# Performance work log

Measured on AMD Instinct MI355X. Metric: run time of the kernel, lower is better.

The kernel has to match this reference:

```python
import jax, jax.numpy as jnp
import numpy as np

N_NODES = 100000
N_EDGES = 3200000
C, H, F = 512, 256, 64


def spmm(edge_row, edge_col, edge_val, Z):
    # (A @ Z)[i] = sum over edges e with row[e]==i of val[e] * Z[col[e]]
    msgs = edge_val[:, None] * Z[edge_col]  # [E, d]
    return jax.ops.segment_sum(msgs, edge_row, num_segments=N_NODES)


def setup_inputs() -> dict:
    key = jax.random.key(0)
    k1, k2, k3, k4, k5, k6, k7 = jax.random.split(key, 7)
    X = jax.random.normal(k1, (N_NODES, C), dtype=jnp.float32)
    edge_row = jax.random.randint(k2, (N_EDGES,), 0, N_NODES, dtype=jnp.int32)
    edge_col = jax.random.randint(k3, (N_EDGES,), 0, N_NODES, dtype=jnp.int32)
    edge_val = jax.random.uniform(k4, (N_EDGES,), dtype=jnp.float32)
    W0 = jax.random.normal(k5, (C, H), dtype=jnp.float32) * (C ** -0.5)
    Wh1 = jax.random.normal(k6, (H, H), dtype=jnp.float32) * (H ** -0.5)
    W1 = jax.random.normal(k7, (H, F), dtype=jnp.float32) * (H ** -0.5)
    return {"X": X, "edge_row": edge_row, "edge_col": edge_col,
            "edge_val": edge_val, "W0": W0, "Wh1": Wh1, "W1": W1}


def reference(X, edge_row, edge_col, edge_val, W0, Wh1, W1):
    # layer 0: relu(A @ (X W0))   (dropout=0 -> identity)
    Z = jax.nn.relu(spmm(edge_row, edge_col, edge_val, X @ W0))
    # hidden layers (num_layers - 2 = 1)
    Z = jax.nn.relu(spmm(edge_row, edge_col, edge_val, Z @ Wh1))
    # output layer: softmax(A @ (Z W1), axis=-1)
    Z = jax.nn.softmax(spmm(edge_row, edge_col, edge_val, Z @ W1), axis=-1)
    return Z
```

## Files before the change

### kernel.cpp

```cpp
#include <hip/hip_runtime.h>
#include <cstdint>
#include <cstddef>


#define SCAN_B 1024

typedef __attribute__((ext_vector_type(8))) short short8_t;
typedef __attribute__((ext_vector_type(4))) short short4_t;
typedef __attribute__((ext_vector_type(4))) float f32x4;

__device__ __forceinline__ short bf16_hi(float x) {
    union { float f; unsigned u; } c; c.f = x;
    return (short)(c.u >> 16);
}
__device__ __forceinline__ float bf16_f32(short h) {
    union { float f; unsigned u; } c; c.u = ((unsigned)(unsigned short)h) << 16;
    return c.f;
}

__device__ __forceinline__ void gload_lds16(const void* g, void* l) {
    __builtin_amdgcn_global_load_lds(
        (const __attribute__((address_space(1))) void*)g,
        (__attribute__((address_space(3))) void*)l, 16, 0, 0);
}


__global__ void count_rows_k(const int* __restrict__ row, int* __restrict__ deg, int E) {
    int e = blockIdx.x * blockDim.x + threadIdx.x;
    if (e < E) atomicAdd(&deg[row[e]], 1);
}

__global__ __launch_bounds__(SCAN_B) void scan1_k(const int* __restrict__ deg,
                                                  int* __restrict__ part,
                                                  int* __restrict__ bsum, int n) {
    __shared__ int buf[SCAN_B];
    int tid = threadIdx.x;
    int i = blockIdx.x * SCAN_B + tid;
    int v = (i < n) ? ((deg[i] + 3) & ~3) : 0;
    buf[tid] = v;
    __syncthreads();
    for (int off = 1; off < SCAN_B; off <<= 1) {
        int y = (tid >= off) ? buf[tid - off] : 0;
        __syncthreads();
        buf[tid] += y;
        __syncthreads();
    }
    if (i < n) part[i] = buf[tid] - v;
    if (tid == SCAN_B - 1) bsum[blockIdx.x] = buf[tid];
}

__global__ __launch_bounds__(128) void scan2_k(int* __restrict__ bsum, int nb) {
    __shared__ int buf[128];
    int tid = threadIdx.x;
    int v = (tid < nb) ? bsum[tid] : 0;
    buf[tid] = v;
    __syncthreads();
    for (int off = 1; off < 128; off <<= 1) {
        int y = (tid >= off) ? buf[tid - off] : 0;
        __syncthreads();
        buf[tid] += y;
        __syncthreads();
    }
    if (tid < nb) bsum[tid] = buf[tid] - v;
    if (tid == nb - 1) bsum[nb] = buf[tid];
}

__global__ __launch_bounds__(SCAN_B) void scan3_k(int* __restrict__ rowptr,
                                                  const int* __restrict__ bsum,
                                                  int* __restrict__ cursor, int n, int nb) {
    int i = blockIdx.x * SCAN_B + threadIdx.x;
    if (i < n) {
        int v = rowptr[i] + bsum[blockIdx.x];
        rowptr[i] = v;
        cursor[i] = v;
    }
    if (i == 0) rowptr[n] = bsum[nb];
}

__global__ __launch_bounds__(256) void scatter_xcd_k(const int* __restrict__ row,
                                                     const int* __restrict__ col,
                                                     const float* __restrict__ val,
                                                     int* __restrict__ cursor,
                                                     int2* __restrict__ ecv,
                                                     int E, int gsz) {
    const int g = blockIdx.x & 7;
    const int rank = blockIdx.x >> 3;
    const int R = gridDim.x >> 3;
    const int lo = g * gsz, hi = lo + gsz;
    for (int e = rank * 256 + threadIdx.x; e < E; e += R * 256) {
        int r = row[e];
        if (r >= lo && r < hi) {
            int p = atomicAdd(&cursor[r], 1);
            ecv[p] = make_int2(col[e], __float_as_int(val[e]));
        }
    }
}


__global__ void split_w_k(const float* __restrict__ W, short* __restrict__ Bhl,
                          int K, int M) {
    int i = blockIdx.x * 256 + threadIdx.x;
    if (i >= K * M) return;
    int k = i / M, m = i - k * M;
    float x = W[i];
    short hi = bf16_hi(x);
    float r = x - bf16_f32(hi);
    short lo = bf16_hi(r);
    int g = k >> 3, j = k & 7;
    Bhl[(size_t)m * (2 * K) + 16 * g + j] = hi;
    Bhl[(size_t)m * (2 * K) + 16 * g + 8 + j] = lo;
}


template <int K, int BN, int NWR, int NWC, bool AF32>
__global__ __launch_bounds__(256) void gemm_hl(const void* __restrict__ Av,
                                               const short* __restrict__ Bhl,
                                               short* __restrict__ ZQ,
                                               float* __restrict__ scl, int N) {
    constexpr int BM = 64 * NWR;
    constexpr int NF = BN / NWC / 16;
    constexpr int NT = K / 32;
    __shared__ short Ald[2][BM * 64];
    __shared__ short Bld[2][BN * 64];

    const int tid = threadIdx.x, lane = tid & 63, w = tid >> 6;
    const int wr = w / NWC, wc = w % NWC;
    const int row0 = blockIdx.x * BM;
    const int l8 = lane >> 3;
    const int sx = (lane & 7) ^ l8;

    const short* Ahl = (const short*)Av;
    const float* Af  = (const float*)Av;
    const int arow = tid >> 2, aq = tid & 3;
    const int akey = arow & 7;

    f32x4 acc[4][NF] = {};

    auto stageB = [&](int t, int b) {
#pragma unroll
        for (int ch = w; ch < BN / 8; ch += 4)
            gload_lds16(Bhl + (size_t)(ch * 8 + l8) * (2 * K) + (size_t)t * 64 + sx * 8,
                        &Bld[b][ch * 512]);
    };
    auto stageAg = [&](int t, int b) {
#pragma unroll
        for (int ch = w; ch < BM / 8; ch += 4)
            gload_lds16(Ahl + (size_t)(row0 + ch * 8 + l8) * (2 * K) + (size_t)t * 64 + sx * 8,
                        &Ald[b][ch * 512]);
    };
    auto loadAf = [&](int t, float4& x0, float4& x1) {
        int gr = row0 + arow;
        x0 = make_float4(0.f, 0.f, 0.f, 0.f); x1 = x0;
        if (gr < N) {
            x0 = *(const float4*)&Af[(size_t)gr * K + t * 32 + aq * 8];
            x1 = *(const float4*)&Af[(size_t)gr * K + t * 32 + aq * 8 + 4];
        }
    };
    auto writeAf = [&](int b, float4 x0, float4 x1) {
        float f[8] = {x0.x, x0.y, x0.z, x0.w, x1.x, x1.y, x1.z, x1.w};
        short8_t hi, lo;
#pragma unroll
        for (int j = 0; j < 8; ++j) {
            short hh = bf16_hi(f[j]);
            hi[j] = hh;
            lo[j] = bf16_hi(f[j] - bf16_f32(hh));
        }
        *(short8_t*)&Ald[b][arow * 64 + ((2 * aq) ^ akey) * 8] = hi;
        *(short8_t*)&Ald[b][arow * 64 + ((2 * aq + 1) ^ akey) * 8] = lo;
    };

    if constexpr (AF32) {
        float4 x0, x1;
        loadAf(0, x0, x1);
        writeAf(0, x0, x1);
    } else {
        stageAg(0, 0);
    }
    stageB(0, 0);
    __syncthreads();

    for (int t = 0; t < NT; ++t) {
        const int cur = t & 1, nxt = cur ^ 1;
        float4 px0, px1;
        if (t + 1 < NT) {
            if constexpr (AF32) loadAf(t + 1, px0, px1);
            else                stageAg(t + 1, nxt);
            stageB(t + 1, nxt);
        }

        const int sH = (lane >> 4) * 2, sL = sH + 1;
        short8_t ah[4], al[4];
#pragma unroll
        for (int m = 0; m < 4; ++m) {
            int rl = wr * 64 + m * 16 + (lane & 15);
            int key = rl & 7;
            ah[m] = *(const short8_t*)&Ald[cur][rl * 64 + (sH ^ key) * 8];
            al[m] = *(const short8_t*)&Ald[cur][rl * 64 + (sL ^ key) * 8];
        }
#pragma unroll
        for (int n = 0; n < NF; ++n) {
            int cl = wc * (BN / NWC) + n * 16 + (lane & 15);
            int key = cl & 7;
            short8_t bh = *(const short8_t*)&Bld[cur][cl * 64 + (sH ^ key) * 8];
            short8_t bl = *(const short8_t*)&Bld[cur][cl * 64 + (sL ^ key) * 8];
#pragma unroll
            for (int m = 0; m < 4; ++m) {
                acc[m][n] = __builtin_amdgcn_mfma_f32_16x16x32_bf16(ah[m], bh, acc[m][n], 0, 0, 0);
                acc[m][n] = __builtin_amdgcn_mfma_f32_16x16x32_bf16(ah[m], bl, acc[m][n], 0, 0, 0);
                acc[m][n] = __builtin_amdgcn_mfma_f32_16x16x32_bf16(al[m], bh, acc[m][n], 0, 0, 0);
            }
        }
        if constexpr (AF32) {
            if (t + 1 < NT) writeAf(nxt, px0, px1);
        }
        __syncthreads();
    }

    const int lg = lane >> 4, lc = lane & 15;
    float* maxb = (float*)&Ald[0][0];
    float rmax[4][4];
#pragma unroll
    for (int m = 0; m < 4; ++m)
#pragma unroll
        for (int r = 0; r < 4; ++r) {
            float v = 0.f;
#pragma unroll
            for (int n = 0; n < NF; ++n) v = fmaxf(v, fabsf(acc[m][n][r]));
#pragma unroll
            for (int o = 8; o >= 1; o >>= 1) v = fmaxf(v, __shfl_xor(v, o));
            rmax[m][r] = v;
        }
    if constexpr (NWC > 1) {
        if (lc == 0)
#pragma unroll
            for (int m = 0; m < 4; ++m)
#pragma unroll
                for (int r = 0; r < 4; ++r)
                    maxb[(wr * 64 + m * 16 + lg * 4 + r) * NWC + wc] = rmax[m][r];
        __syncthreads();
    }
#pragma unroll
    for (int m = 0; m < 4; ++m)
#pragma unroll
        for (int r = 0; r < 4; ++r) {
            int rl = wr * 64 + m * 16 + lg * 4 + r;
            float v = rmax[m][r];
            if constexpr (NWC > 1) {
                v = maxb[rl * NWC];
#pragma unroll
                for (int q = 1; q < NWC; ++q) v = fmaxf(v, maxb[rl * NWC + q]);
            }
            int grow = row0 + rl;
            if (grow < N) {
                float inv = (v > 0.f) ? 32767.f / v : 0.f;
                if (lc == 0 && wc == 0) scl[grow] = v * (1.f / 32767.f);
#pragma unroll
                for (int n = 0; n < NF; ++n)
                    ZQ[(size_t)grow * BN + wc * (BN / NWC) + n * 16 + lc] =
                        (short)rintf(acc[m][n][r] * inv);
            }
        }
}


__global__ __launch_bounds__(256) void spmm_agg256_k(const int* __restrict__ rowptr,
                                                     const int2* __restrict__ ecv,
                                                     const short* __restrict__ Q,
                                                     const float* __restrict__ scl,
                                                     short* __restrict__ Zhl, int N) {
    int row = blockIdx.x * 4 + (threadIdx.x >> 6);
    if (row >= N) return;
    const int lane = threadIdx.x & 63;
    const int half = lane >> 5;
    const int l32 = lane & 31;
    int s = rowptr[row], e = rowptr[row + 1];
    const short8_t* Qv = (const short8_t*)Q;
    f32x4 a0 = {0.f, 0.f, 0.f, 0.f}, a1 = a0;
    for (int i = s; i < e; i += 4) {
        int4 A = *(const int4*)(ecv + i);
        int4 B = *(const int4*)(ecv + i + 2);
        int   cA = half ? A.z : A.x;
        float wA = __int_as_float(half ? A.w : A.y) * scl[cA];
        int   cB = half ? B.z : B.x;
        float wB = __int_as_float(half ? B.w : B.y) * scl[cB];
        short8_t qA = Qv[(size_t)cA * 32 + l32];
        short8_t qB = Qv[(size_t)cB * 32 + l32];
#pragma unroll
        for (int j = 0; j < 4; ++j) {
            a0[j] = fmaf(wA, (float)qA[j], a0[j]);
            a1[j] = fmaf(wA, (float)qA[j + 4], a1[j]);
            a0[j] = fmaf(wB, (float)qB[j], a0[j]);
            a1[j] = fmaf(wB, (float)qB[j + 4], a1[j]);
        }
    }
#pragma unroll
    for (int j = 0; j < 4; ++j) {
        a0[j] += __shfl_xor(a0[j], 32);
        a1[j] += __shfl_xor(a1[j], 32);
    }
    if (half == 0) {
        short8_t hi, lo;
#pragma unroll
        for (int j = 0; j < 4; ++j) {
            float r0 = fmaxf(a0[j], 0.f), r1 = fmaxf(a1[j], 0.f);
            short h0 = bf16_hi(r0), h1 = bf16_hi(r1);
            hi[j] = h0; hi[j + 4] = h1;
            lo[j] = bf16_hi(r0 - bf16_f32(h0));
            lo[j + 4] = bf16_hi(r1 - bf16_f32(h1));
        }
        size_t base = (size_t)row * 512 + l32 * 16;
        *(short8_t*)&Zhl[base] = hi;
        *(short8_t*)&Zhl[base + 8] = lo;
    }
}

__global__ __launch_bounds__(256) void spmm_softmax64_k(const int* __restrict__ rowptr,
                                                        const int2* __restrict__ ecv,
                                                        const short* __restrict__ Q,
                                                        const float* __restrict__ scl,
                                                        float* __restrict__ out, int N) {
    int row = blockIdx.x * 4 + (threadIdx.x >> 6);
    if (row >= N) return;
    const int lane = threadIdx.x & 63;
    const int q = lane >> 4;
    const int l16 = lane & 15;
    int s = rowptr[row], e = rowptr[row + 1];
    const short4_t* Qv = (const short4_t*)Q;
    f32x4 acc = {0.f, 0.f, 0.f, 0.f};
    for (int i = s; i < e; i += 4) {
        int4 A = *(const int4*)(ecv + i);
        int4 B = *(const int4*)(ecv + i + 2);
        int c = (q & 2) ? ((q & 1) ? B.z : B.x) : ((q & 1) ? A.z : A.x);
        int wbits = (q & 2) ? ((q & 1) ? B.w : B.y) : ((q & 1) ? A.w : A.y);
        float wv = __int_as_float(wbits) * scl[c];
        short4_t z = Qv[(size_t)c * 16 + l16];
#pragma unroll
        for (int j = 0; j < 4; ++j) acc[j] = fmaf(wv, (float)z[j], acc[j]);
    }
#pragma unroll
    for (int j = 0; j < 4; ++j) {
        acc[j] += __shfl_xor(acc[j], 16);
        acc[j] += __shfl_xor(acc[j], 32);
    }
    float m = fmaxf(fmaxf(acc[0], acc[1]), fmaxf(acc[2], acc[3]));
#pragma unroll
    for (int o = 8; o >= 1; o >>= 1) m = fmaxf(m, __shfl_xor(m, o));
    float p0 = __expf(acc[0] - m), p1 = __expf(acc[1] - m);
    float p2 = __expf(acc[2] - m), p3 = __expf(acc[3] - m);
    float ssum = p0 + p1 + p2 + p3;
#pragma unroll
    for (int o = 8; o >= 1; o >>= 1) ssum += __shfl_xor(ssum, o);
    if (q == 0) {
        float inv = 1.f / ssum;
        float4 o4 = make_float4(p0 * inv, p1 * inv, p2 * inv, p3 * inv);
        *(float4*)&out[(size_t)row * 64 + l16 * 4] = o4;
    }
}


extern "C" void kernel_launch(void* const* d_in, const int* in_sizes, int n_in,
                              void* d_out, int out_size, void* d_ws, size_t ws_size,
                              hipStream_t stream) {
    const float* X        = (const float*)d_in[0];
    const int*   edge_row = (const int*)d_in[1];
    const int*   edge_col = (const int*)d_in[2];
    const float* edge_val = (const float*)d_in[3];
    const float* W0       = (const float*)d_in[4];
    const float* Wh1      = (const float*)d_in[5];
    const float* W1       = (const float*)d_in[6];

    const int C = 512, H = 256, F = 64;
    const int N = in_sizes[0] / C;
    const int E = in_sizes[1];
    const int EPAD = E + 4 * N + 64;

    size_t off = 0;
    auto alloc = [&](size_t bytes) -> void* {
        void* p = (char*)d_ws + off;
        off += (bytes + 255) & ~(size_t)255;
        return p;
    };
    short* Zhl    = (short*)alloc((size_t)N * 2 * H * sizeof(short));
    short* ZQ     = (short*)alloc((size_t)N * H * sizeof(short));
    float* scl    = (float*)alloc((size_t)N * sizeof(float));
    int*   deg    = (int*)alloc((size_t)N * sizeof(int));
    int*   rowptr = (int*)alloc((size_t)(N + 1) * sizeof(int));
    int*   cursor = (int*)alloc((size_t)N * sizeof(int));
    int*   bsum   = (int*)alloc(129 * sizeof(int));
    int2*  ecv    = (int2*)alloc((size_t)EPAD * sizeof(int2));
    short* Bhl0   = (short*)alloc((size_t)H * 2 * C * sizeof(short));
    short* Bhl1   = (short*)alloc((size_t)H * 2 * H * sizeof(short));
    short* Bhl2   = (short*)alloc((size_t)F * 2 * H * sizeof(short));
    (void)ws_size;

    hipMemsetAsync(deg, 0, (size_t)N * sizeof(int), stream);
    hipMemsetAsync(ecv, 0, (size_t)EPAD * sizeof(int2), stream);
    count_rows_k<<<(E + 255) / 256, 256, 0, stream>>>(edge_row, deg, E);
    int nb = (N + SCAN_B - 1) / SCAN_B;
    scan1_k<<<nb, SCAN_B, 0, stream>>>(deg, rowptr, bsum, N);
    scan2_k<<<1, 128, 0, stream>>>(bsum, nb);
    scan3_k<<<nb, SCAN_B, 0, stream>>>(rowptr, bsum, cursor, N, nb);
    const int gsz = (N + 7) / 8;
    scatter_xcd_k<<<8 * 256, 256, 0, stream>>>(edge_row, edge_col, edge_val,
                                               cursor, ecv, E, gsz);

    split_w_k<<<(C * H + 255) / 256, 256, 0, stream>>>(W0, Bhl0, C, H);
    split_w_k<<<(H * H + 255) / 256, 256, 0, stream>>>(Wh1, Bhl1, H, H);
    split_w_k<<<(H * F + 255) / 256, 256, 0, stream>>>(W1, Bhl2, H, F);

    const int g64  = (N + 63) / 64;
    const int g128 = (N + 127) / 128;
    const int rg   = (N + 3) / 4;

    gemm_hl<512, 256, 1, 4, true><<<g64, 256, 0, stream>>>(X, Bhl0, ZQ, scl, N);
    spmm_agg256_k<<<rg, 256, 0, stream>>>(rowptr, ecv, ZQ, scl, Zhl, N);
    gemm_hl<256, 256, 1, 4, false><<<g64, 256, 0, stream>>>(Zhl, Bhl1, ZQ, scl, N);
    spmm_agg256_k<<<rg, 256, 0, stream>>>(rowptr, ecv, ZQ, scl, Zhl, N);
    gemm_hl<256, 64, 2, 2, false><<<g128, 256, 0, stream>>>(Zhl, Bhl2, ZQ, scl, N);
    spmm_softmax64_k<<<rg, 256, 0, stream>>>(rowptr, ecv, ZQ, scl,
                                             (float*)d_out, N);
}
```

Baseline: 1.124 ms.

## Deepen GEMM prefetch pipeline with explicit vmcnt waits and raw barriers

Restructures the dense GEMM main loop so global loads for tile t+2 (and fp32 A for t+3) are issued ahead, using fine-grained s_waitcnt vmcnt and s_barrier instead of __syncthreads. The goal is to keep more memory traffic in flight behind the MFMA work and to avoid full wait-all barriers. It depends on hand-counted vmcnt values matching the compiler's emitted load count, which is fragile, and the extra prefetch registers may raise register pressure. A __syncthreads is added before the cross-wave max reduction to keep LDS reuse safe.

```diff
diff --git a/kernel.cpp b/kernel.cpp
--- a/kernel.cpp
+++ b/kernel.cpp
@@ -22,6 +22,18 @@
     __builtin_amdgcn_global_load_lds(
         (const __attribute__((address_space(1))) void*)g,
         (__attribute__((address_space(3))) void*)l, 16, 0, 0);
+}
+
+#define GBAR() asm volatile("s_barrier" ::: "memory")
+#define LGKM0() asm volatile("s_waitcnt lgkmcnt(0)" ::: "memory")
+
+__device__ __forceinline__ void wait_vm(int n) {
+    switch (n) {
+        case 0:  asm volatile("s_waitcnt vmcnt(0)"  ::: "memory"); break;
+        case 6:  asm volatile("s_waitcnt vmcnt(6)"  ::: "memory"); break;
+        case 8:  asm volatile("s_waitcnt vmcnt(8)"  ::: "memory"); break;
+        default: asm volatile("s_waitcnt vmcnt(10)" ::: "memory"); break;
+    }
 }
 
 
@@ -120,6 +132,9 @@
     constexpr int BM = 64 * NWR;
     constexpr int NF = BN / NWC / 16;
     constexpr int NT = K / 32;
+    constexpr int LB = BN / 8 / 4;
+    constexpr int LA = AF32 ? 0 : BM / 8 / 4;
+    constexpr int L  = LA + LB;
     __shared__ short Ald[2][BM * 64];
     __shared__ short Bld[2][BN * 64];
 
@@ -169,40 +184,40 @@
         *(short8_t*)&Ald[b][arow * 64 + ((2 * aq + 1) ^ akey) * 8] = lo;
     };
 
+    float4 pxa[2], pxb[2];
     if constexpr (AF32) {
-        float4 x0, x1;
-        loadAf(0, x0, x1);
-        writeAf(0, x0, x1);
+        float4 a0, a1, b0, b1;
+        loadAf(0, a0, a1); stageB(0, 0); writeAf(0, a0, a1);
+        loadAf(1, b0, b1); stageB(1, 1); writeAf(1, b0, b1);
+        loadAf(2, pxa[0], pxb[0]);
+        wait_vm(10);
+        LGKM0();
     } else {
-        stageAg(0, 0);
-    }
-    stageB(0, 0);
-    __syncthreads();
-
+        stageAg(0, 0); stageB(0, 0);
+        stageAg(1, 1); stageB(1, 1);
+        wait_vm(L);
+    }
+    GBAR();
+
+#pragma unroll
     for (int t = 0; t < NT; ++t) {
-        const int cur = t & 1, nxt = cur ^ 1;
-        float4 px0, px1;
-        if (t + 1 < NT) {
-            if constexpr (AF32) loadAf(t + 1, px0, px1);
-            else                stageAg(t + 1, nxt);
-            stageB(t + 1, nxt);
-        }
-
-        const int sH = (lane >> 4) * 2, sL = sH + 1;
+        const int cur = t & 1;
+
+        const int sH = (lane >> 4) * 2, sL2 = sH + 1;
         short8_t ah[4], al[4];
 #pragma unroll
         for (int m = 0; m < 4; ++m) {
             int rl = wr * 64 + m * 16 + (lane & 15);
             int key = rl & 7;
             ah[m] = *(const short8_t*)&Ald[cur][rl * 64 + (sH ^ key) * 8];
-            al[m] = *(const short8_t*)&Ald[cur][rl * 64 + (sL ^ key) * 8];
+            al[m] = *(const short8_t*)&Ald[cur][rl * 64 + (sL2 ^ key) * 8];
         }
 #pragma unroll
         for (int n = 0; n < NF; ++n) {
             int cl = wc * (BN / NWC) + n * 16 + (lane & 15);
             int key = cl & 7;
             short8_t bh = *(const short8_t*)&Bld[cur][cl * 64 + (sH ^ key) * 8];
-            short8_t bl = *(const short8_t*)&Bld[cur][cl * 64 + (sL ^ key) * 8];
+            short8_t bl = *(const short8_t*)&Bld[cur][cl * 64 + (sL2 ^ key) * 8];
 #pragma unroll
             for (int m = 0; m < 4; ++m) {
                 acc[m][n] = __builtin_amdgcn_mfma_f32_16x16x32_bf16(ah[m], bh, acc[m][n], 0, 0, 0);
@@ -210,10 +225,21 @@
                 acc[m][n] = __builtin_amdgcn_mfma_f32_16x16x32_bf16(al[m], bh, acc[m][n], 0, 0, 0);
             }
         }
+
+        GBAR();
         if constexpr (AF32) {
-            if (t + 1 < NT) writeAf(nxt, px0, px1);
-        }
-        __syncthreads();
+            if (t + 3 < NT) loadAf(t + 3, pxa[(t + 1) & 1], pxb[(t + 1) & 1]);
+            if (t + 2 < NT) {
+                stageB(t + 2, cur);
+                writeAf(cur, pxa[t & 1], pxb[t & 1]);
+            }
+            LGKM0();
+            wait_vm((t + 3 < NT ? 2 : 0) + (t + 2 < NT ? LB : 0));
+        } else {
+            if (t + 2 < NT) { stageAg(t + 2, cur); stageB(t + 2, cur); }
+            wait_vm(t + 2 < NT ? L : 0);
+        }
+        GBAR();
     }
 
     const int lg = lane >> 4, lc = lane & 15;
@@ -231,6 +257,7 @@
             rmax[m][r] = v;
         }
     if constexpr (NWC > 1) {
+        __syncthreads();
         if (lc == 0)
 #pragma unroll
             for (int m = 0; m < 4; ++m)
```

Result: no change. 1.122 ms (-0.2%).
